# Performance work log

Measured on AMD Instinct MI355X. Metric: run time of the kernel, lower is better.

The kernel has to match this reference:

```python
import jax, jax.numpy as jnp
import numpy as np

N = 4096
D_IMG = 512
D_FEAT = 512
D_H = 256
D_Z = 128
N_CLS = 64
CHANGE_FRAC = 1.0  # alpha


def setup_inputs() -> dict:
    key = jax.random.key(0)
    ks = jax.random.split(key, 12)
    u = jax.random.uniform(ks[0], (N, N))
    a = (jnp.triu(u, 1) < 0.01).astype(jnp.float32)
    adj_ori = a + a.T
    i = jnp.arange(N)
    # GCN-normalized adjacency D^-1/2 (A+I) D^-1/2 (input to ep_net)
    a_hat = adj_ori.at[i, i].set(1.0)
    d = jnp.power(a_hat.sum(1), -0.5)
    adj_norm = a_hat * d[:, None] * d[None, :]
    xav = lambda k, s: jax.random.uniform(k, s, jnp.float32, -1.0, 1.0) * jnp.sqrt(6.0 / (s[0] + s[1]))
    return {
        "adj_norm": adj_norm,
        "adj_ori": adj_ori,
        "feats_ori": jax.random.normal(ks[1], (N, D_FEAT), jnp.float32),
        "img_feats": jax.random.normal(ks[2], (N, D_IMG), jnp.float32),
        "csd_ori": jax.random.normal(ks[3], (N_CLS, D_FEAT), jnp.float32),
        "csd_img": jax.random.normal(ks[4], (N_CLS, D_IMG), jnp.float32),
        "noise": jax.random.normal(ks[5], (N, D_Z), jnp.float32),
        "Wb": xav(ks[6], (D_IMG, D_H)),
        "Wm": xav(ks[7], (D_H, D_Z)),
        "Wl": xav(ks[8], (D_H, D_Z)),
        "fc1_W": xav(ks[9], (2 * D_FEAT, D_H)),
        "fc1_b": jnp.zeros((D_H,), jnp.float32),
        "fc2_W": xav(ks[10], (2 * D_H, D_IMG)),
        "fc2_b": jnp.zeros((D_IMG,), jnp.float32),
    }


def _ceil_st(x):
    # CeilNoGradient: ceil forward, identity backward (straight-through)
    return x + jax.lax.stop_gradient(jnp.ceil(x) - x)


def _gsage_layer(adj, h, W, b, relu):
    neigh = adj @ h
    mean_neigh = neigh / (adj.sum(axis=1, keepdims=True) + 1e-7)
    x = jnp.concatenate((h, mean_neigh), axis=1) @ W + b
    return jax.nn.relu(x) if relu else x


def _sample_adj_edge(adj_logits, adj):
    n_edges = jnp.sum(adj != 0)
    n_change = jnp.floor(n_edges.astype(jnp.float32) * CHANGE_FRAC / 2.0).astype(jnp.int32)
    ep = jnp.triu(adj_logits, 1)
    ep = ep - jnp.min(ep)
    ep = ep / jnp.max(ep)
    T = N * N
    # --- remove lowest-prob existing edges ---
    mask_rm = ep * adj
    v = jnp.sort(mask_rm.reshape(-1))  # ascending; positives at the tail
    n_nz = jnp.sum(v > 0)
    n_rm = jnp.minimum(n_nz, n_change)
    thresh_rm = v[T - n_nz + n_rm - 1]  # n_rm-th smallest positive
    mask_rm = jnp.where(mask_rm > thresh_rm, 0.0, mask_rm)
    mask_rm = _ceil_st(mask_rm)
    mask_rm = mask_rm + mask_rm.T
    adj_new = adj - mask_rm
    # --- add highest-prob missing edges ---
    mask_add = ep * (1.0 - adj)
    v2 = jnp.sort(mask_add.reshape(-1))
    n_nz2 = jnp.sum(v2 > 0)
    n_add = jnp.minimum(n_nz2, n_change)
    thresh_add = v2[T - n_add]  # n_add-th largest positive
    mask_add = jnp.where(mask_add < thresh_add, 0.0, mask_add)
    mask_add = _ceil_st(mask_add)
    mask_add = mask_add + mask_add.T
    return adj_new + mask_add


def reference(adj_norm, adj_ori, feats_ori, img_feats, csd_ori, csd_img, noise,
              Wb, Wm, Wl, fc1_W, fc1_b, fc2_W, fc2_b):
    # ep_net (VGAE, gae=False)
    hidden = adj_norm @ (img_feats @ Wb)
    mean = jax.nn.relu(adj_norm @ (hidden @ Wm))
    logstd = jax.nn.relu(adj_norm @ (hidden @ Wl))
    Z = noise * jnp.exp(logstd) + mean
    adj_logits = Z @ Z.T
    # edge rewiring
    adj_new = _sample_adj_edge(adj_logits, adj_ori)
    # normalize_adj for 'gsage': fill diag 1, L1 row-normalize
    i = jnp.arange(N)
    adj_new = adj_new.at[i, i].set(1.0)
    adj_new = adj_new / jnp.maximum(jnp.sum(jnp.abs(adj_new), axis=1, keepdims=True), 1e-12)
    # nc_net (DGPN)
    preds_img = img_feats @ csd_img.T
    h1 = _gsage_layer(adj_new, feats_ori, fc1_W, fc1_b, relu=True)
    h2 = _gsage_layer(adj_new, h1, fc2_W, fc2_b, relu=False)
    feat_total = jax.nn.log_softmax(h2, axis=-1)
    preds_total = feat_total @ csd_img.T
    return preds_total, feat_total, preds_img, adj_logits
```

## Files before the change

kernel.cpp:

```cpp
#include <hip/hip_runtime.h>
#include <type_traits>
#include <stdint.h>

#define NN 4096
#define TTOT 16777216UL

enum { F_RELU=1, F_ACC=2, F_RS=4, F_BIAS=8 };

typedef unsigned short ushort_t;
using bf16x8 = __attribute__((ext_vector_type(8))) short;
using f32x4  = __attribute__((ext_vector_type(4))) float;

struct SelParams {
  unsigned min_ord, max_ord, n_up;
  float lo, M, c0;
  unsigned n_change, rm_prefix, rm_k, add_prefix, add_k;
  float t_rm, t_add;
  unsigned hist_rm[256], hist_add[256];
};

__device__ __forceinline__ unsigned ordenc(float x){
  unsigned u = __float_as_uint(x);
  return (u & 0x80000000u) ? ~u : (u | 0x80000000u);
}
__device__ __forceinline__ float orddec_ok(unsigned o){
  unsigned u = (o & 0x80000000u) ? (o ^ 0x80000000u) : ~o;
  return __uint_as_float(u);
}
__device__ __forceinline__ ushort_t f2bf(float x){
  unsigned u = __float_as_uint(x);
  return (ushort_t)((u + 0x7FFFu + ((u >> 16) & 1u)) >> 16);
}
__device__ __forceinline__ float bf2f(ushort_t h){
  return __uint_as_float(((unsigned)h) << 16);
}

template<int DN>
__global__ __launch_bounds__(256)
void k_b3t(const float* __restrict__ Bsrc, ushort_t* __restrict__ H,
           ushort_t* __restrict__ Mg, ushort_t* __restrict__ L)
{
  __shared__ ushort_t sh[64][65], sm[64][65], sl[64][65];
  const int t = threadIdx.x;
  const int n0 = blockIdx.x * 64, k0 = blockIdx.y * 64;
  #pragma unroll
  for (int it = 0; it < 16; ++it){
    int idx = it*256 + t; int r = idx >> 6, c = idx & 63;
    float x  = Bsrc[(size_t)(k0 + r)*DN + n0 + c];
    ushort_t hb = f2bf(x);
    float r1 = x - bf2f(hb);
    ushort_t mb = f2bf(r1);
    float r2 = r1 - bf2f(mb);
    ushort_t lb = f2bf(r2);
    sh[r][c] = hb; sm[r][c] = mb; sl[r][c] = lb;
  }
  __syncthreads();
  #pragma unroll
  for (int it = 0; it < 16; ++it){
    int idx = it*256 + t; int r = idx >> 6, c = idx & 63;
    size_t o = (size_t)(n0 + r)*4096 + k0 + c;
    H[o] = sh[c][r]; Mg[o] = sm[c][r]; L[o] = sl[c][r];
  }
}

__global__ __launch_bounds__(256)
void k_mfma(const signed char* __restrict__ A8,
            const ushort_t* __restrict__ BH, const ushort_t* __restrict__ BM2,
            const ushort_t* __restrict__ BL,
            float* __restrict__ C0, float* __restrict__ C1, int N)
{
  __shared__ ushort_t Ab[64][72];
  __shared__ ushort_t Bb[3][64][72];
  const int t = threadIdx.x;
  const int m0 = blockIdx.y * 64, n0 = blockIdx.x * 64;
  const int kz = blockIdx.z;
  const int kbase = kz * 2048;
  float* C = kz ? C1 : C0;
  const int sr = t >> 2, sc = (t & 3) * 16;
  const int w = t >> 6, lane = t & 63;
  const int fr = lane & 15, fg = lane >> 4;

  int4 a_r = *reinterpret_cast<const int4*>(A8 + (size_t)(m0+sr)*4096 + kbase + sc);
  const ushort_t* bsrc0 = BH  + (size_t)(n0+sr)*4096 + kbase + sc;
  const ushort_t* bsrc1 = BM2 + (size_t)(n0+sr)*4096 + kbase + sc;
  const ushort_t* bsrc2 = BL  + (size_t)(n0+sr)*4096 + kbase + sc;
  int4 b0a = reinterpret_cast<const int4*>(bsrc0)[0], b0b = reinterpret_cast<const int4*>(bsrc0)[1];
  int4 b1a = reinterpret_cast<const int4*>(bsrc1)[0], b1b = reinterpret_cast<const int4*>(bsrc1)[1];
  int4 b2a = reinterpret_cast<const int4*>(bsrc2)[0], b2b = reinterpret_cast<const int4*>(bsrc2)[1];

  f32x4 acc[4][3];
  #pragma unroll
  for (int c = 0; c < 4; ++c)
    #pragma unroll
    for (int p = 0; p < 3; ++p)
      acc[c][p] = (f32x4){0.f, 0.f, 0.f, 0.f};

  for (int k0 = 0; k0 < 2048; k0 += 64){
    {
      alignas(16) ushort_t tmp[16];
      const signed char* ab = reinterpret_cast<const signed char*>(&a_r);
      #pragma unroll
      for (int i = 0; i < 16; ++i) tmp[i] = f2bf((float)(int)ab[i]);
      *reinterpret_cast<int4*>(&Ab[sr][sc])     = reinterpret_cast<int4*>(tmp)[0];
      *reinterpret_cast<int4*>(&Ab[sr][sc + 8]) = reinterpret_cast<int4*>(tmp)[1];
      *reinterpret_cast<int4*>(&Bb[0][sr][sc])     = b0a;
      *reinterpret_cast<int4*>(&Bb[0][sr][sc + 8]) = b0b;
      *reinterpret_cast<int4*>(&Bb[1][sr][sc])     = b1a;
      *reinterpret_cast<int4*>(&Bb[1][sr][sc + 8]) = b1b;
      *reinterpret_cast<int4*>(&Bb[2][sr][sc])     = b2a;
      *reinterpret_cast<int4*>(&Bb[2][sr][sc + 8]) = b2b;
    }
    __syncthreads();
    if (k0 + 64 < 2048){
      a_r = *reinterpret_cast<const int4*>(A8 + (size_t)(m0+sr)*4096 + kbase + (k0+64) + sc);
      const ushort_t* p0 = BH  + (size_t)(n0+sr)*4096 + kbase + (k0+64) + sc;
      const ushort_t* p1 = BM2 + (size_t)(n0+sr)*4096 + kbase + (k0+64) + sc;
      const ushort_t* p2 = BL  + (size_t)(n0+sr)*4096 + kbase + (k0+64) + sc;
      b0a = reinterpret_cast<const int4*>(p0)[0]; b0b = reinterpret_cast<const int4*>(p0)[1];
      b1a = reinterpret_cast<const int4*>(p1)[0]; b1b = reinterpret_cast<const int4*>(p1)[1];
      b2a = reinterpret_cast<const int4*>(p2)[0]; b2b = reinterpret_cast<const int4*>(p2)[1];
    }
    #pragma unroll
    for (int kk = 0; kk < 64; kk += 32){
      bf16x8 af = *reinterpret_cast<const bf16x8*>(&Ab[w*16 + fr][kk + fg*8]);
      #pragma unroll
      for (int c = 0; c < 4; ++c){
        const int bn = c*16 + fr;
        bf16x8 bh = *reinterpret_cast<const bf16x8*>(&Bb[0][bn][kk + fg*8]);
        acc[c][0] = __builtin_amdgcn_mfma_f32_16x16x32_bf16(af, bh, acc[c][0], 0, 0, 0);
        bf16x8 bm = *reinterpret_cast<const bf16x8*>(&Bb[1][bn][kk + fg*8]);
        acc[c][1] = __builtin_amdgcn_mfma_f32_16x16x32_bf16(af, bm, acc[c][1], 0, 0, 0);
        bf16x8 bl = *reinterpret_cast<const bf16x8*>(&Bb[2][bn][kk + fg*8]);
        acc[c][2] = __builtin_amdgcn_mfma_f32_16x16x32_bf16(af, bl, acc[c][2], 0, 0, 0);
      }
    }
    __syncthreads();
  }
  #pragma unroll
  for (int c = 0; c < 4; ++c){
    f32x4 s = acc[c][0] + acc[c][1];
    s = s + acc[c][2];
    #pragma unroll
    for (int r = 0; r < 4; ++r)
      C[(size_t)(m0 + w*16 + fg*4 + r)*N + n0 + c*16 + fr] = s[r];
  }
}

__global__ __launch_bounds__(256)
void k_add2(const float* __restrict__ A, const float* __restrict__ B,
            float* __restrict__ O, int n4)
{
  int i = blockIdx.x*256 + threadIdx.x;
  if (i < n4){
    float4 a = reinterpret_cast<const float4*>(A)[i];
    float4 b = reinterpret_cast<const float4*>(B)[i];
    reinterpret_cast<float4*>(O)[i] = make_float4(a.x+b.x, a.y+b.y, a.z+b.z, a.w+b.w);
  }
}

__global__ __launch_bounds__(256)
void k_z2p(const float* __restrict__ MPLP, const float* __restrict__ noise,
           ushort_t* __restrict__ ZH, ushort_t* __restrict__ ZM,
           ushort_t* __restrict__ ZL)
{
  int i = blockIdx.x*256 + threadIdx.x;
  int m = i >> 7, c = i & 127;
  float mp = fmaxf(MPLP[(size_t)m*256 + c], 0.0f);
  float lp = fmaxf(MPLP[(size_t)m*256 + 128 + c], 0.0f);
  float z = noise[i]*expf(lp) + mp;
  ushort_t hb = f2bf(z);
  float r1 = z - bf2f(hb);
  ushort_t mb = f2bf(r1);
  float r2 = r1 - bf2f(mb);
  ushort_t lb = f2bf(r2);
  ZH[i] = hb; ZM[i] = mb; ZL[i] = lb;
}

__global__ __launch_bounds__(256)
void k_zztm(const ushort_t* __restrict__ ZH, const ushort_t* __restrict__ ZM,
            const ushort_t* __restrict__ ZL, float* __restrict__ C)
{
  const int bx = blockIdx.x, by = blockIdx.y;
  if (by > bx) return;
  __shared__ float Cs[64][68];
  const int t = threadIdx.x;
  const int m0 = by*64, n0 = bx*64;
  const int w = t >> 6, lane = t & 63;
  const int fr = lane & 15, fg = lane >> 4;
  const int arow = m0 + w*16 + fr;

  f32x4 acc[4];
  #pragma unroll
  for (int c = 0; c < 4; ++c) acc[c] = (f32x4){0.f,0.f,0.f,0.f};

  #pragma unroll
  for (int kk = 0; kk < 128; kk += 32){
    bf16x8 ah = *reinterpret_cast<const bf16x8*>(ZH + (size_t)arow*128 + kk + fg*8);
    bf16x8 am = *reinterpret_cast<const bf16x8*>(ZM + (size_t)arow*128 + kk + fg*8);
    bf16x8 al = *reinterpret_cast<const bf16x8*>(ZL + (size_t)arow*128 + kk + fg*8);
    #pragma unroll
    for (int c = 0; c < 4; ++c){
      const int brow = n0 + c*16 + fr;
      bf16x8 bh = *reinterpret_cast<const bf16x8*>(ZH + (size_t)brow*128 + kk + fg*8);
      bf16x8 bm = *reinterpret_cast<const bf16x8*>(ZM + (size_t)brow*128 + kk + fg*8);
      bf16x8 bl = *reinterpret_cast<const bf16x8*>(ZL + (size_t)brow*128 + kk + fg*8);
      acc[c] = __builtin_amdgcn_mfma_f32_16x16x32_bf16(ah, bh, acc[c], 0, 0, 0);
      acc[c] = __builtin_amdgcn_mfma_f32_16x16x32_bf16(ah, bm, acc[c], 0, 0, 0);
      acc[c] = __builtin_amdgcn_mfma_f32_16x16x32_bf16(am, bh, acc[c], 0, 0, 0);
      acc[c] = __builtin_amdgcn_mfma_f32_16x16x32_bf16(ah, bl, acc[c], 0, 0, 0);
      acc[c] = __builtin_amdgcn_mfma_f32_16x16x32_bf16(al, bh, acc[c], 0, 0, 0);
      acc[c] = __builtin_amdgcn_mfma_f32_16x16x32_bf16(am, bm, acc[c], 0, 0, 0);
    }
  }
  #pragma unroll
  for (int c = 0; c < 4; ++c)
    #pragma unroll
    for (int r = 0; r < 4; ++r)
      Cs[w*16 + fg*4 + r][c*16 + fr] = acc[c][r];
  __syncthreads();
  const int rr = t >> 2, cb = (t & 3) * 16;
  #pragma unroll
  for (int j = 0; j < 4; ++j){
    float4 v = *reinterpret_cast<const float4*>(&Cs[rr][cb + j*4]);
    *reinterpret_cast<float4*>(&C[(size_t)(m0+rr)*NN + n0 + cb + j*4]) = v;
  }
  if (bx != by){
    #pragma unroll
    for (int j = 0; j < 4; ++j){
      float4 v = make_float4(Cs[cb+j*4+0][rr], Cs[cb+j*4+1][rr],
                             Cs[cb+j*4+2][rr], Cs[cb+j*4+3][rr]);
      *reinterpret_cast<float4*>(&C[(size_t)(n0+rr)*NN + m0 + cb + j*4]) = v;
    }
  }
}

template<typename TA>
__global__ __launch_bounds__(256)
void k_gemm32(const TA* __restrict__ A, const float* __restrict__ B,
              float* __restrict__ C, int M, int N, int K, int ldc,
              const float* __restrict__ rowscale, const float* __restrict__ bias,
              int flags)
{
  __shared__ float As[16][36];
  __shared__ float Bs[16][68];
  const int t  = threadIdx.x;
  const int tx = t & 15, ty = t >> 4;
  const int m0 = blockIdx.y * 32, n0 = blockIdx.x * 64;
  float acc[2][4] = {};
  for (int k0 = 0; k0 < K; k0 += 16) {
    if (t < 128){
      const int mA = t >> 2, kA = (t & 3) * 4;
      if constexpr (std::is_same<TA, float>::value) {
        float4 v = *reinterpret_cast<const float4*>(A + (size_t)(m0+mA)*K + (k0+kA));
        As[kA+0][mA]=v.x; As[kA+1][mA]=v.y; As[kA+2][mA]=v.z; As[kA+3][mA]=v.w;
      } else {
        int u = *reinterpret_cast<const int*>(A + (size_t)(m0+mA)*K + (k0+kA));
        As[kA+0][mA]=(float)(int)(signed char)( u       & 0xff);
        As[kA+1][mA]=(float)(int)(signed char)((u>>8)   & 0xff);
        As[kA+2][mA]=(float)(int)(signed char)((u>>16)  & 0xff);
        As[kA+3][mA]=(float)(int)(signed char)((u>>24)  & 0xff);
      }
    }
    {
      const int kB = t >> 4, nB = (t & 15) * 4;
      float4 w = *reinterpret_cast<const float4*>(B + (size_t)(k0+kB)*N + (n0+nB));
      Bs[kB][nB+0]=w.x; Bs[kB][nB+1]=w.y; Bs[kB][nB+2]=w.z; Bs[kB][nB+3]=w.w;
    }
    __syncthreads();
    #pragma unroll
    for (int kk = 0; kk < 16; ++kk) {
      float a0 = As[kk][ty*2+0];
      float a1 = As[kk][ty*2+1];
      float4 bv = *reinterpret_cast<const float4*>(&Bs[kk][tx*4]);
      float b[4]={bv.x,bv.y,bv.z,bv.w};
      #pragma unroll
      for (int j=0;j<4;++j){
        acc[0][j] = fmaf(a0, b[j], acc[0][j]);
        acc[1][j] = fmaf(a1, b[j], acc[1][j]);
      }
    }
    __syncthreads();
  }
  #pragma unroll
  for (int i=0;i<2;++i){
    const int m = m0 + ty*2 + i;
    const float rsv = (flags & F_RS) ? rowscale[m] : 1.0f;
    float* cp = C + (size_t)m*ldc + (n0 + tx*4);
    float o[4];
    #pragma unroll
    for (int j=0;j<4;++j){
      float v = acc[i][j] * rsv;
      if (flags & F_BIAS) v += bias[n0 + tx*4 + j];
      if (flags & F_ACC)  v += cp[j];
      if (flags & F_RELU) v = fmaxf(v, 0.0f);
      o[j] = v;
    }
    *reinterpret_cast<float4*>(cp) = make_float4(o[0],o[1],o[2],o[3]);
  }
}

__global__ __launch_bounds__(256)
void k_gemm32T(const float* __restrict__ A, const float* __restrict__ B,
               float* __restrict__ C, int M, int N, int K, int ldc)
{
  __shared__ float As[16][36];
  __shared__ float Bs[16][68];
  const int t  = threadIdx.x;
  const int tx = t & 15, ty = t >> 4;
  const int m0 = blockIdx.y * 32, n0 = blockIdx.x * 64;
  float acc[2][4] = {};
  for (int k0 = 0; k0 < K; k0 += 16) {
    if (t < 128){
      const int mA = t >> 2, kA = (t & 3) * 4;
      float4 v = *reinterpret_cast<const float4*>(A + (size_t)(m0+mA)*K + (k0+kA));
      As[kA+0][mA]=v.x; As[kA+1][mA]=v.y; As[kA+2][mA]=v.z; As[kA+3][mA]=v.w;
    }
    {
      const int nB = t >> 2, kB = (t & 3) * 4;
      float4 w = *reinterpret_cast<const float4*>(B + (size_t)(n0+nB)*K + (k0+kB));
      Bs[kB+0][nB]=w.x; Bs[kB+1][nB]=w.y; Bs[kB+2][nB]=w.z; Bs[kB+3][nB]=w.w;
    }
    __syncthreads();
    #pragma unroll
    for (int kk = 0; kk < 16; ++kk) {
      float a0 = As[kk][ty*2+0];
      float a1 = As[kk][ty*2+1];
      float4 bv = *reinterpret_cast<const float4*>(&Bs[kk][tx*4]);
      float b[4]={bv.x,bv.y,bv.z,bv.w};
      #pragma unroll
      for (int j=0;j<4;++j){
        acc[0][j] = fmaf(a0, b[j], acc[0][j]);
        acc[1][j] = fmaf(a1, b[j], acc[1][j]);
      }
    }
    __syncthreads();
  }
  #pragma unroll
  for (int i=0;i<2;++i){
    const int m = m0 + ty*2 + i;
    float* cp = C + (size_t)m*ldc + (n0 + tx*4);
    *reinterpret_cast<float4*>(cp) = make_float4(acc[i][0],acc[i][1],acc[i][2],acc[i][3]);
  }
}

__global__ __launch_bounds__(256)
void k_fc(const float* __restrict__ A1, const float* __restrict__ B1,
          const float* __restrict__ bias,
          const float* __restrict__ A2, const float* __restrict__ B2,
          const float* __restrict__ rowscale,
          float* __restrict__ C, int N, int K1, int K2, int relu)
{
  __shared__ float As[16][36];
  __shared__ float Bs[16][68];
  const int t  = threadIdx.x;
  const int tx = t & 15, ty = t >> 4;
  const int m0 = blockIdx.y * 32, n0 = blockIdx.x * 64;
  float acc1[2][4] = {};
  float acc2[2][4] = {};
  for (int k0 = 0; k0 < K1; k0 += 16) {
    if (t < 128){
      const int mA = t >> 2, kA = (t & 3) * 4;
      float4 v = *reinterpret_cast<const float4*>(A1 + (size_t)(m0+mA)*K1 + (k0+kA));
      As[kA+0][mA]=v.x; As[kA+1][mA]=v.y; As[kA+2][mA]=v.z; As[kA+3][mA]=v.w;
    }
    {
      const int kB = t >> 4, nB = (t & 15) * 4;
      float4 w = *reinterpret_cast<const float4*>(B1 + (size_t)(k0+kB)*N + (n0+nB));
      Bs[kB][nB+0]=w.x; Bs[kB][nB+1]=w.y; Bs[kB][nB+2]=w.z; Bs[kB][nB+3]=w.w;
    }
    __syncthreads();
    #pragma unroll
    for (int kk = 0; kk < 16; ++kk) {
      float a0 = As[kk][ty*2+0];
      float a1 = As[kk][ty*2+1];
      float4 bv = *reinterpret_cast<const float4*>(&Bs[kk][tx*4]);
      float b[4]={bv.x,bv.y,bv.z,bv.w};
      #pragma unroll
      for (int j=0;j<4;++j){
        acc1[0][j] = fmaf(a0, b[j], acc1[0][j]);
        acc1[1][j] = fmaf(a1, b[j], acc1[1][j]);
      }
    }
    __syncthreads();
  }
  for (int k0 = 0; k0 < K2; k0 += 16) {
    if (t < 128){
      const int mA = t >> 2, kA = (t & 3) * 4;
      float4 v = *reinterpret_cast<const float4*>(A2 + (size_t)(m0+mA)*K2 + (k0+kA));
      As[kA+0][mA]=v.x; As[kA+1][mA]=v.y; As[kA+2][mA]=v.z; As[kA+3][mA]=v.w;
    }
    {
      const int kB = t >> 4, nB = (t & 15) * 4;
      float4 w = *reinterpret_cast<const float4*>(B2 + (size_t)(k0+kB)*N + (n0+nB));
      Bs[kB][nB+0]=w.x; Bs[kB][nB+1]=w.y; Bs[kB][nB+2]=w.z; Bs[kB][nB+3]=w.w;
    }
    __syncthreads();
    #pragma unroll
    for (int kk = 0; kk < 16; ++kk) {
      float a0 = As[kk][ty*2+0];
      float a1 = As[kk][ty*2+1];
      float4 bv = *reinterpret_cast<const float4*>(&Bs[kk][tx*4]);
      float b[4]={bv.x,bv.y,bv.z,bv.w};
      #pragma unroll
      for (int j=0;j<4;++j){
        acc2[0][j] = fmaf(a0, b[j], acc2[0][j]);
        acc2[1][j] = fmaf(a1, b[j], acc2[1][j]);
      }
    }
    __syncthreads();
  }
  #pragma unroll
  for (int i=0;i<2;++i){
    const int m = m0 + ty*2 + i;
    const float rsv = rowscale[m];
    float* cp = C + (size_t)m*N + (n0 + tx*4);
    float o[4];
    #pragma unroll
    for (int j=0;j<4;++j){
      float t1 = acc1[i][j] + bias[n0 + tx*4 + j];
      float v  = acc2[i][j] * rsv;
      v += t1;
      if (relu) v = fmaxf(v, 0.0f);
      o[j] = v;
    }
    *reinterpret_cast<float4*>(cp) = make_float4(o[0],o[1],o[2],o[3]);
  }
}

__global__ __launch_bounds__(256)
void k_wcat(const float* __restrict__ Wm, const float* __restrict__ Wl,
            float* __restrict__ Wcat)
{
  int idx = blockIdx.x*256 + threadIdx.x;
  int row = idx >> 8, col = idx & 255;
  Wcat[idx] = (col < 128) ? Wm[row*128 + col] : Wl[row*128 + (col - 128)];
}

template<int D>
__global__ __launch_bounds__(256)
void k_spmmF(const float* __restrict__ A, const float* __restrict__ B,
             float* __restrict__ C)
{
  const int row = blockIdx.x, t = threadIdx.x;
  const int lane = t & 63, wv = t >> 6;
  __shared__ int   sc[288];
  __shared__ float sv[288];
  __shared__ int wtot[4];
  __shared__ int nsh;
  const float4* r4 = reinterpret_cast<const float4*>(A + (size_t)row*NN) + t*4;
  float lv[16];
  #pragma unroll
  for (int q=0;q<4;++q){
    float4 v = r4[q];
    lv[q*4+0]=v.x; lv[q*4+1]=v.y; lv[q*4+2]=v.z; lv[q*4+3]=v.w;
  }
  int c = 0;
  #pragma unroll
  for (int k=0;k<16;++k) c += (lv[k] != 0.0f);
  int inc = c;
  #pragma unroll
  for (int off=1; off<64; off<<=1){
    int v = __shfl_up(inc, off, 64);
    if (lane >= off) inc += v;
  }
  if (lane == 63) wtot[wv] = inc;
  __syncthreads();
  int wbase = 0;
  #pragma unroll
  for (int ww=0; ww<3; ++ww) if (ww < wv) wbase += wtot[ww];
  int pos = wbase + inc - c;
  #pragma unroll
  for (int k=0;k<16;++k){
    if (lv[k] != 0.0f){
      if (pos >= 0 && pos < 288){ sc[pos] = t*16+k; sv[pos] = lv[k]; }
      pos++;
    }
  }
  if (t == 255){
    int tot = wbase + inc;
    nsh = (tot < 288) ? tot : 288;
  }
  __syncthreads();
  const int n = nsh;
  float acc = 0.f;
  int s = 0;
  for (; s+4 <= n; s += 4){
    float x0 = B[(size_t)sc[s+0]*D + t];
    float x1 = B[(size_t)sc[s+1]*D + t];
    float x2 = B[(size_t)sc[s+2]*D + t];
    float x3 = B[(size_t)sc[s+3]*D + t];
    acc = fmaf(sv[s+0], x0, acc);
    acc = fmaf(sv[s+1], x1, acc);
    acc = fmaf(sv[s+2], x2, acc);
    acc = fmaf(sv[s+3], x3, acc);
  }
  for (; s < n; ++s) acc = fmaf(sv[s], B[(size_t)sc[s]*D + t], acc);
  C[(size_t)row*D + t] = acc;
}

__global__ __launch_bounds__(256)
void k_initstats(SelParams* p)
{
  int t = threadIdx.x;
  if (t == 0){
    p->min_ord = 0xFFFFFFFFu; p->max_ord = 0u; p->n_up = 0u;
    p->rm_prefix = 0u; p->add_prefix = 0u;
  }
  p->hist_rm[t] = 0u; p->hist_add[t] = 0u;
}

__global__ __launch_bounds__(256)
void k_stats1(const float* __restrict__ L, const float* __restrict__ adj,
              unsigned long long* __restrict__ mask, SelParams* __restrict__ p)
{
  unsigned mn=0xFFFFFFFFu, mx=0u, cnt=0u;
  size_t g = (size_t)blockIdx.x*256 + threadIdx.x;
  const size_t stride = (size_t)gridDim.x*256;
  for (; g < 262144; g += stride){
    const int i  = (int)(g >> 6);
    const int jb = (int)(g & 63) << 6;
    unsigned long long m = 0ull;
    if (jb + 63 > i){
      const float4* a4 = reinterpret_cast<const float4*>(adj + (size_t)i*NN + jb);
      const float4* l4 = reinterpret_cast<const float4*>(L   + (size_t)i*NN + jb);
      for (int w = 0; w < 16; ++w){
        const int j0 = jb + w*4;
        if (j0 + 3 <= i) continue;
        float4 av = a4[w]; float4 lv = l4[w];
        float ae[4]={av.x,av.y,av.z,av.w};
        float le[4]={lv.x,lv.y,lv.z,lv.w};
        #pragma unroll
        for (int e=0;e<4;++e){
          const int jj = j0 + e;
          if (jj > i){
            if (ae[e] != 0.0f){ m |= 1ull << (jj & 63); cnt++; }
            unsigned o = ordenc(le[e]);
            mn = (o < mn) ? o : mn;
            mx = (o > mx) ? o : mx;
          }
        }
      }
    }
    mask[g] = m;
  }
  __shared__ unsigned smn[256], smx[256], sc[256];
  int t = threadIdx.x;
  smn[t]=mn; smx[t]=mx; sc[t]=cnt; __syncthreads();
  for (int s=128; s>0; s>>=1){
    if (t < s){
      smn[t] = (smn[t+s] < smn[t]) ? smn[t+s] : smn[t];
      smx[t] = (smx[t+s] > smx[t]) ? smx[t+s] : smx[t];
      sc[t] += sc[t+s];
    }
    __syncthreads();
  }
  if (t == 0){
    atomicMin(&p->min_ord, smn[0]);
    atomicMax(&p->max_ord, smx[0]);
    atomicAdd(&p->n_up, sc[0]);
  }
}

__global__ void k_stats2(SelParams* p)
{
  float mnv = orddec_ok(p->min_ord), mxv = orddec_ok(p->max_ord);
  float lo = fminf(mnv, 0.0f), hi = fmaxf(mxv, 0.0f);
  p->lo = lo;
  p->M  = hi - lo;
  p->c0 = (0.0f - lo) / p->M;
  p->n_change = p->n_up;
}

__global__ __launch_bounds__(256)
void k_hist2(const float* __restrict__ L, const unsigned long long* __restrict__ mask,
             SelParams* __restrict__ p, int shift)
{
  __shared__ unsigned hr[256], ha[256];
  const int t = threadIdx.x;
  hr[t]=0u; ha[t]=0u; __syncthreads();
  const float lo = p->lo, Mv = p->M;
  const unsigned pr = p->rm_prefix, pa = p->add_prefix;
  const float4* L4 = reinterpret_cast<const float4*>(L);
  size_t q = (size_t)blockIdx.x*256 + t;
  const size_t stride = (size_t)gridDim.x*256;
  for (; q < TTOT/4; q += stride){
    const int i = (int)(q >> 10);
    const int j = (int)(q & 1023) << 2;
    if (j + 3 <= i) continue;
    float4 l = L4[q];
    const unsigned long long w = mask[q >> 4];
    float le[4]={l.x,l.y,l.z,l.w};
    #pragma unroll
    for (int e=0;e<4;++e){
      const int jj = j + e;
      if (jj <= i) continue;
      const unsigned key = __float_as_uint((le[e] - lo) / Mv);
      if (key == 0u) continue;
      const bool edge = (w >> (jj & 63)) & 1ull;
      if (edge){
        if (shift == 24 || (key >> (shift+8)) == pr) atomicAdd(&hr[(key>>shift)&255u], 1u);
      } else {
        if (shift == 24 || (key >> (shift+8)) == pa) atomicAdd(&ha[(key>>shift)&255u], 1u);
      }
    }
  }
  __syncthreads();
  if (hr[t]) atomicAdd(&p->hist_rm[t], hr[t]);
  if (ha[t]) atomicAdd(&p->hist_add[t], ha[t]);
}

__global__ __launch_bounds__(256)
void k_scan2(SelParams* __restrict__ p, int shift)
{
  const int t = threadIdx.x;
  if (t == 0){
    const unsigned c0k  = __float_as_uint(p->c0);
    const unsigned n_up = p->n_up;
    {
      unsigned injb = 300u, inj = 0u;
      if (c0k != 0u && (shift == 24 || (c0k >> (shift+8)) == p->rm_prefix)){
        injb = (c0k >> shift) & 255u; inj = n_up;
      }
      unsigned k;
      if (shift == 24){
        unsigned tot = inj;
        for (int d=0; d<256; ++d) tot += p->hist_rm[d];
        k = (tot < p->n_change) ? tot : p->n_change;
      } else k = p->rm_k;
      unsigned cum = 0u, digit = 255u;
      for (int d=0; d<256; ++d){
        unsigned hd = p->hist_rm[d] + (((unsigned)d == injb) ? inj : 0u);
        if (cum + hd >= k){ digit = (unsigned)d; k -= cum; break; }
        cum += hd;
      }
      p->rm_prefix = (p->rm_prefix << 8) | digit;
      p->rm_k = k;
      if (shift == 0) p->t_rm = __uint_as_float(p->rm_prefix);
    }
    {
      unsigned injb = 300u, inj = 0u;
      if (c0k != 0u && (shift == 24 || (c0k >> (shift+8)) == p->add_prefix)){
        injb = (c0k >> shift) & 255u;
        inj  = 8386560u - n_up + 4096u;
      }
      unsigned k;
      if (shift == 24){
        unsigned tot = inj;
        for (int d=0; d<256; ++d) tot += p->hist_add[d];
        k = (tot < p->n_change) ? tot : p->n_change;
      } else k = p->add_k;
      unsigned cum = 0u, digit = 0u;
      for (int d=255; d>=0; --d){
        unsigned hd = p->hist_add[d] + (((unsigned)d == injb) ? inj : 0u);
        if (cum + hd >= k){ digit = (unsigned)d; k -= cum; break; }
        cum += hd;
      }
      p->add_prefix = (p->add_prefix << 8) | digit;
      p->add_k = k;
      if (shift == 0) p->t_add = __uint_as_float(p->add_prefix);
    }
  }
  __syncthreads();
  p->hist_rm[t] = 0u; p->hist_add[t] = 0u;
}

__device__ __forceinline__ int adjval(bool edge, float v, float c0v, float trm, float tad)
{
  int rmU = (edge && v   >  0.0f && v   <= trm) ? 1 : 0;
  int rmL = (edge && c0v >  0.0f && c0v <= trm) ? 1 : 0;
  int adU = (!edge && v   >= tad) ? 1 : 0;
  int adL = (!edge && c0v >= tad) ? 1 : 0;
  return (edge ? 1 : 0) - rmU - rmL + adU + adL;
}

__global__ __launch_bounds__(256)
void k_apply(const float* __restrict__ L, const unsigned long long* __restrict__ mask,
             const SelParams* __restrict__ p, signed char* __restrict__ A8)
{
  const int bx = blockIdx.x, by = blockIdx.y;
  if (by > bx) return;
  const float lo=p->lo, Mv=p->M, c0v=p->c0, trm=p->t_rm, tad=p->t_add;
  const int i0 = by*64, j0 = bx*64, t = threadIdx.x;
  __shared__ signed char Vs[64][65];
  if (bx == by){
    for (int it=0; it<16; ++it){
      int e = it*256 + t; int r = e>>6, c = e&63;
      size_t idx = (size_t)(i0+r)*NN + (j0+c);
      if (r < c){
        bool edge = (mask[idx>>6] >> ((j0+c) & 63)) & 1ull;
        float v = (L[idx] - lo) / Mv;
        int val = adjval(edge, v, c0v, trm, tad);
        A8[idx] = (signed char)val;
        Vs[c][r] = (signed char)val;
      } else if (r == c){
        A8[idx] = 1;
      }
    }
    __syncthreads();
    for (int it=0; it<16; ++it){
      int e = it*256 + t; int r = e>>6, c = e&63;
      if (r > c) A8[(size_t)(i0+r)*NN + (j0+c)] = Vs[r][c];
    }
  } else {
    for (int it=0; it<16; ++it){
      int e = it*256 + t; int r = e>>6, c = e&63;
      size_t idx = (size_t)(i0+r)*NN + (j0+c);
      bool edge = (mask[idx>>6] >> ((j0+c) & 63)) & 1ull;
      float v = (L[idx] - lo) / Mv;
      int val = adjval(edge, v, c0v, trm, tad);
      A8[idx] = (signed char)val;
      Vs[c][r] = (signed char)val;
    }
    __syncthreads();
    for (int it=0; it<16; ++it){
      int e = it*256 + t; int r = e>>6, c = e&63;
      A8[(size_t)(j0+r)*NN + (i0+c)] = Vs[r][c];
    }
  }
}

__global__ __launch_bounds__(256)
void k_rowsum8(const signed char* __restrict__ A8, float* __restrict__ s_mean)
{
  const int row = blockIdx.x, t = threadIdx.x;
  const int4 w = reinterpret_cast<const int4*>(A8 + (size_t)row*NN)[t];
  int s = 0, a = 0;
  int vs[4] = {w.x, w.y, w.z, w.w};
  #pragma unroll
  for (int q=0; q<4; ++q){
    int u = vs[q];
    #pragma unroll
    for (int b=0; b<4; ++b){
      int c = (int)(signed char)((u >> (8*b)) & 0xff);
      s += c; a += (c < 0) ? -c : c;
    }
  }
  __shared__ int rs_[256], ra_[256];
  rs_[t]=s; ra_[t]=a; __syncthreads();
  for (int st=128; st>0; st>>=1){
    if (t < st){ rs_[t]+=rs_[t+st]; ra_[t]+=ra_[t+st]; }
    __syncthreads();
  }
  if (t == 0){
    float rs = (float)rs_[0], ra = (float)ra_[0];
    float A = fmaxf(ra, 1e-12f);
    s_mean[row] = (1.0f / A) / (rs / A + 1e-7f);
  }
}

__global__ __launch_bounds__(256)
void k_lsm(float* __restrict__ X)
{
  const int row = blockIdx.x, t = threadIdx.x;
  float* x = X + (size_t)row*512;
  float v0 = x[t], v1 = x[t+256];
  __shared__ float red[256];
  red[t] = fmaxf(v0, v1); __syncthreads();
  for (int s=128; s>0; s>>=1){
    if (t < s) red[t] = fmaxf(red[t], red[t+s]);
    __syncthreads();
  }
  float m = red[0]; __syncthreads();
  red[t] = expf(v0-m) + expf(v1-m); __syncthreads();
  for (int s=128; s>0; s>>=1){
    if (t < s) red[t] += red[t+s];
    __syncthreads();
  }
  float ls = logf(red[0]);
  x[t]     = (v0 - m) - ls;
  x[t+256] = (v1 - m) - ls;
}

extern "C" void kernel_launch(void* const* d_in, const int* in_sizes, int n_in,
                              void* d_out, int out_size, void* d_ws, size_t ws_size,
                              hipStream_t stream)
{
  (void)in_sizes; (void)n_in; (void)out_size; (void)ws_size;
  const float* adj_norm = (const float*)d_in[0];
  const float* adj_ori  = (const float*)d_in[1];
  const float* feats    = (const float*)d_in[2];
  const float* img      = (const float*)d_in[3];
  const float* csd_img  = (const float*)d_in[5];
  const float* noise    = (const float*)d_in[6];
  const float* Wb       = (const float*)d_in[7];
  const float* Wm       = (const float*)d_in[8];
  const float* Wl       = (const float*)d_in[9];
  const float* fc1W     = (const float*)d_in[10];
  const float* fc1b     = (const float*)d_in[11];
  const float* fc2W     = (const float*)d_in[12];
  const float* fc2b     = (const float*)d_in[13];

  float* out    = (float*)d_out;
  float* out_pt = out;
  float* out_ft = out + 262144;
  float* out_pi = out + 2359296;
  float* out_lg = out + 2621440;

  char* W = (char*)d_ws;
  signed char* adj8 = (signed char*)W;
  float* bufA   = (float*)(W + (16u<<20));
  float* bufB   = (float*)(W + (24u<<20));
  float* HMHL   = (float*)(W + (28u<<20));
  float* MPLP   = (float*)(W + (32u<<20));
  unsigned long long* mask = (unsigned long long*)(W + (38u<<20));
  float* p2q0   = (float*)(W + (40u<<20));
  float* s_mean = (float*)(W + (44u<<20));
  SelParams* sp = (SelParams*)(W + (44u<<20) + 65536);
  float* Wcat   = (float*)(W + (45u<<20));
  ushort_t* ZH = (ushort_t*)(W + (40u<<20));
  ushort_t* ZM = (ushort_t*)(W + (41u<<20));
  ushort_t* ZL = (ushort_t*)(W + (42u<<20));
  ushort_t* BT1h = (ushort_t*)(W + (28u<<20));
  ushort_t* BT1m = (ushort_t*)(W + (32u<<20));
  ushort_t* BT1l = (ushort_t*)(W + (36u<<20));
  ushort_t* BT2h = (ushort_t*)(W + (28u<<20));
  ushort_t* BT2m = (ushort_t*)(W + (30u<<20));
  ushort_t* BT2l = (ushort_t*)(W + (32u<<20));

  dim3 B(256);
  auto G32 = [](int M, int N){ return dim3((unsigned)(N/64), (unsigned)(M/32)); };

  k_gemm32<float><<<G32(4096,256),B,0,stream>>>(img, Wb, bufA, 4096,256,512,256, nullptr,nullptr,0);
  k_spmmF<256><<<4096,B,0,stream>>>(adj_norm, bufA, bufB);
  k_wcat<<<256,B,0,stream>>>(Wm, Wl, Wcat);
  k_gemm32<float><<<G32(4096,256),B,0,stream>>>(bufB, Wcat, HMHL, 4096,256,256,256, nullptr,nullptr,0);
  k_spmmF<256><<<4096,B,0,stream>>>(adj_norm, HMHL, MPLP);
  k_z2p<<<2048,B,0,stream>>>(MPLP, noise, ZH, ZM, ZL);
  k_zztm<<<dim3(64,64),B,0,stream>>>(ZH, ZM, ZL, out_lg);

  k_initstats<<<1,B,0,stream>>>(sp);
  k_stats1<<<1024,B,0,stream>>>(out_lg, adj_ori, mask, sp);
  k_stats2<<<1,1,0,stream>>>(sp);
  for (int shift = 24; shift >= 0; shift -= 8){
    k_hist2<<<2048,B,0,stream>>>(out_lg, mask, sp, shift);
    k_scan2<<<1,B,0,stream>>>(sp, shift);
  }
  k_apply<<<dim3(64,64),B,0,stream>>>(out_lg, mask, sp, adj8);

  k_rowsum8<<<4096,B,0,stream>>>(adj8, s_mean);

  k_b3t<512><<<dim3(8,64),B,0,stream>>>(feats, BT1h, BT1m, BT1l);
  k_mfma<<<dim3(8,64,2),B,0,stream>>>(adj8, BT1h, BT1m, BT1l, bufA, out_ft, 512);
  k_add2<<<2048,B,0,stream>>>(bufA, out_ft, bufA, 524288);
  k_fc<<<G32(4096,256),B,0,stream>>>(feats, fc1W, fc1b, bufA, fc1W + 512*256, s_mean,
                                     bufB, 256, 512, 512, 1);
  k_b3t<256><<<dim3(4,64),B,0,stream>>>(bufB, BT2h, BT2m, BT2l);
  k_mfma<<<dim3(4,64,2),B,0,stream>>>(adj8, BT2h, BT2m, BT2l, p2q0, out_ft, 256);
  k_add2<<<1024,B,0,stream>>>(p2q0, out_ft, bufA, 262144);
  k_fc<<<G32(4096,512),B,0,stream>>>(bufB, fc2W, fc2b, bufA, fc2W + 256*512, s_mean,
                                     out_ft, 512, 256, 256, 0);
  k_lsm<<<4096,B,0,stream>>>(out_ft);

  k_gemm32T<<<G32(4096,64),B,0,stream>>>(out_ft, csd_img, out_pt, 4096,64,512,64);
  k_gemm32T<<<G32(4096,64),B,0,stream>>>(img, csd_img, out_pi, 4096,64,512,64);
}
```

Measured before the change: 906.1 us.

## Stage Z tiles in LDS for ZZ^T and swap warp-to-tile mapping in adj GEMM

The Z·Zᵀ logits kernel now cooperatively loads the 64-row A and B tiles of the three bf16 split components into shared memory, instead of having each wave read B fragments straight from global memory. The epilogue reuses that shared buffer for the transpose stage. The adjacency MFMA kernel swaps its mapping so each wave holds one B column fragment and loops over four A row tiles, which cuts LDS fragment loads per iteration (3 B + 4 A instead of 1 A + 12 B). Both changes aim to reduce redundant memory traffic, at the cost of extra shared memory and barriers in the logits kernel.

Measured after the change: 840.9 us. 1.08x faster.

```diff
diff --git a/kernel.cpp b/kernel.cpp
--- a/kernel.cpp
+++ b/kernel.cpp
@@ -90,10 +90,10 @@
 
   f32x4 acc[4][3];
   #pragma unroll
-  for (int c = 0; c < 4; ++c)
+  for (int mt = 0; mt < 4; ++mt)
     #pragma unroll
     for (int p = 0; p < 3; ++p)
-      acc[c][p] = (f32x4){0.f, 0.f, 0.f, 0.f};
+      acc[mt][p] = (f32x4){0.f, 0.f, 0.f, 0.f};
 
   for (int k0 = 0; k0 < 2048; k0 += 64){
     {
@@ -122,27 +122,27 @@
     }
     #pragma unroll
     for (int kk = 0; kk < 64; kk += 32){
-      bf16x8 af = *reinterpret_cast<const bf16x8*>(&Ab[w*16 + fr][kk + fg*8]);
+      const int bn = w*16 + fr;
+      bf16x8 bh = *reinterpret_cast<const bf16x8*>(&Bb[0][bn][kk + fg*8]);
+      bf16x8 bm = *reinterpret_cast<const bf16x8*>(&Bb[1][bn][kk + fg*8]);
+      bf16x8 bl = *reinterpret_cast<const bf16x8*>(&Bb[2][bn][kk + fg*8]);
       #pragma unroll
-      for (int c = 0; c < 4; ++c){
-        const int bn = c*16 + fr;
-        bf16x8 bh = *reinterpret_cast<const bf16x8*>(&Bb[0][bn][kk + fg*8]);
-        acc[c][0] = __builtin_amdgcn_mfma_f32_16x16x32_bf16(af, bh, acc[c][0], 0, 0, 0);
-        bf16x8 bm = *reinterpret_cast<const bf16x8*>(&Bb[1][bn][kk + fg*8]);
-        acc[c][1] = __builtin_amdgcn_mfma_f32_16x16x32_bf16(af, bm, acc[c][1], 0, 0, 0);
-        bf16x8 bl = *reinterpret_cast<const bf16x8*>(&Bb[2][bn][kk + fg*8]);
-        acc[c][2] = __builtin_amdgcn_mfma_f32_16x16x32_bf16(af, bl, acc[c][2], 0, 0, 0);
-      }
-    }
-    __syncthreads();
-  }
-  #pragma unroll
-  for (int c = 0; c < 4; ++c){
-    f32x4 s = acc[c][0] + acc[c][1];
-    s = s + acc[c][2];
+      for (int mt = 0; mt < 4; ++mt){
+        bf16x8 af = *reinterpret_cast<const bf16x8*>(&Ab[mt*16 + fr][kk + fg*8]);
+        acc[mt][0] = __builtin_amdgcn_mfma_f32_16x16x32_bf16(af, bh, acc[mt][0], 0, 0, 0);
+        acc[mt][1] = __builtin_amdgcn_mfma_f32_16x16x32_bf16(af, bm, acc[mt][1], 0, 0, 0);
+        acc[mt][2] = __builtin_amdgcn_mfma_f32_16x16x32_bf16(af, bl, acc[mt][2], 0, 0, 0);
+      }
+    }
+    __syncthreads();
+  }
+  #pragma unroll
+  for (int mt = 0; mt < 4; ++mt){
+    f32x4 s = acc[mt][0] + acc[mt][1];
+    s = s + acc[mt][2];
     #pragma unroll
     for (int r = 0; r < 4; ++r)
-      C[(size_t)(m0 + w*16 + fg*4 + r)*N + n0 + c*16 + fr] = s[r];
+      C[(size_t)(m0 + mt*16 + fg*4 + r)*N + n0 + w*16 + fr] = s[r];
   }
 }
 
@@ -177,58 +177,89 @@
 }
 
 __global__ __launch_bounds__(256)
-void k_zztm(const ushort_t* __restrict__ ZH, const ushort_t* __restrict__ ZM,
-            const ushort_t* __restrict__ ZL, float* __restrict__ C)
+void k_zztm2(const ushort_t* __restrict__ ZH, const ushort_t* __restrict__ ZM,
+             const ushort_t* __restrict__ ZL, float* __restrict__ C)
 {
   const int bx = blockIdx.x, by = blockIdx.y;
   if (by > bx) return;
-  __shared__ float Cs[64][68];
+  __shared__ ushort_t As[3][64][72];
+  __shared__ ushort_t Bs[3][64][72];
   const int t = threadIdx.x;
   const int m0 = by*64, n0 = bx*64;
+  const int sr = t >> 2, sc = (t & 3) * 16;
   const int w = t >> 6, lane = t & 63;
   const int fr = lane & 15, fg = lane >> 4;
-  const int arow = m0 + w*16 + fr;
 
   f32x4 acc[4];
   #pragma unroll
-  for (int c = 0; c < 4; ++c) acc[c] = (f32x4){0.f,0.f,0.f,0.f};
-
-  #pragma unroll
-  for (int kk = 0; kk < 128; kk += 32){
-    bf16x8 ah = *reinterpret_cast<const bf16x8*>(ZH + (size_t)arow*128 + kk + fg*8);
-    bf16x8 am = *reinterpret_cast<const bf16x8*>(ZM + (size_t)arow*128 + kk + fg*8);
-    bf16x8 al = *reinterpret_cast<const bf16x8*>(ZL + (size_t)arow*128 + kk + fg*8);
-    #pragma unroll
-    for (int c = 0; c < 4; ++c){
-      const int brow = n0 + c*16 + fr;
-      bf16x8 bh = *reinterpret_cast<const bf16x8*>(ZH + (size_t)brow*128 + kk + fg*8);
-      bf16x8 bm = *reinterpret_cast<const bf16x8*>(ZM + (size_t)brow*128 + kk + fg*8);
-      bf16x8 bl = *reinterpret_cast<const bf16x8*>(ZL + (size_t)brow*128 + kk + fg*8);
-      acc[c] = __builtin_amdgcn_mfma_f32_16x16x32_bf16(ah, bh, acc[c], 0, 0, 0);
-      acc[c] = __builtin_amdgcn_mfma_f32_16x16x32_bf16(ah, bm, acc[c], 0, 0, 0);
-      acc[c] = __builtin_amdgcn_mfma_f32_16x16x32_bf16(am, bh, acc[c], 0, 0, 0);
-      acc[c] = __builtin_amdgcn_mfma_f32_16x16x32_bf16(ah, bl, acc[c], 0, 0, 0);
-      acc[c] = __builtin_amdgcn_mfma_f32_16x16x32_bf16(al, bh, acc[c], 0, 0, 0);
-      acc[c] = __builtin_amdgcn_mfma_f32_16x16x32_bf16(am, bm, acc[c], 0, 0, 0);
-    }
-  }
-  #pragma unroll
-  for (int c = 0; c < 4; ++c)
+  for (int mt = 0; mt < 4; ++mt) acc[mt] = (f32x4){0.f,0.f,0.f,0.f};
+
+  for (int k0 = 0; k0 < 128; k0 += 64){
+    const ushort_t* pa0 = ZH + (size_t)(m0+sr)*128 + k0 + sc;
+    const ushort_t* pa1 = ZM + (size_t)(m0+sr)*128 + k0 + sc;
+    const ushort_t* pa2 = ZL + (size_t)(m0+sr)*128 + k0 + sc;
+    const ushort_t* pb0 = ZH + (size_t)(n0+sr)*128 + k0 + sc;
+    const ushort_t* pb1 = ZM + (size_t)(n0+sr)*128 + k0 + sc;
+    const ushort_t* pb2 = ZL + (size_t)(n0+sr)*128 + k0 + sc;
+    int4 a0a = reinterpret_cast<const int4*>(pa0)[0], a0b = reinterpret_cast<const int4*>(pa0)[1];
+    int4 a1a = reinterpret_cast<const int4*>(pa1)[0], a1b = reinterpret_cast<const int4*>(pa1)[1];
+    int4 a2a = reinterpret_cast<const int4*>(pa2)[0], a2b = reinterpret_cast<const int4*>(pa2)[1];
+    int4 b0a = reinterpret_cast<const int4*>(pb0)[0], b0b = reinterpret_cast<const int4*>(pb0)[1];
+    int4 b1a = reinterpret_cast<const int4*>(pb1)[0], b1b = reinterpret_cast<const int4*>(pb1)[1];
+    int4 b2a = reinterpret_cast<const int4*>(pb2)[0], b2b = reinterpret_cast<const int4*>(pb2)[1];
+    __syncthreads();
+    *reinterpret_cast<int4*>(&As[0][sr][sc])     = a0a;
+    *reinterpret_cast<int4*>(&As[0][sr][sc + 8]) = a0b;
+    *reinterpret_cast<int4*>(&As[1][sr][sc])     = a1a;
+    *reinterpret_cast<int4*>(&As[1][sr][sc + 8]) = a1b;
+    *reinterpret_cast<int4*>(&As[2][sr][sc])     = a2a;
+    *reinterpret_cast<int4*>(&As[2][sr][sc + 8]) = a2b;
+    *reinterpret_cast<int4*>(&Bs[0][sr][sc])     = b0a;
+    *reinterpret_cast<int4*>(&Bs[0][sr][sc + 8]) = b0b;
+    *reinterpret_cast<int4*>(&Bs[1][sr][sc])     = b1a;
+    *reinterpret_cast<int4*>(&Bs[1][sr][sc + 8]) = b1b;
+    *reinterpret_cast<int4*>(&Bs[2][sr][sc])     = b2a;
+    *reinterpret_cast<int4*>(&Bs[2][sr][sc + 8]) = b2b;
+    __syncthreads();
+    #pragma unroll
+    for (int kk = 0; kk < 64; kk += 32){
+      const int bn = w*16 + fr;
+      bf16x8 bh = *reinterpret_cast<const bf16x8*>(&Bs[0][bn][kk + fg*8]);
+      bf16x8 bm = *reinterpret_cast<const bf16x8*>(&Bs[1][bn][kk + fg*8]);
+      bf16x8 bl = *reinterpret_cast<const bf16x8*>(&Bs[2][bn][kk + fg*8]);
+      #pragma unroll
+      for (int mt = 0; mt < 4; ++mt){
+        bf16x8 ah = *reinterpret_cast<const bf16x8*>(&As[0][mt*16 + fr][kk + fg*8]);
+        bf16x8 am = *reinterpret_cast<const bf16x8*>(&As[1][mt*16 + fr][kk + fg*8]);
+        bf16x8 al = *reinterpret_cast<const bf16x8*>(&As[2][mt*16 + fr][kk + fg*8]);
+        acc[mt] = __builtin_amdgcn_mfma_f32_16x16x32_bf16(ah, bh, acc[mt], 0, 0, 0);
+        acc[mt] = __builtin_amdgcn_mfma_f32_16x16x32_bf16(ah, bm, acc[mt], 0, 0, 0);
+        acc[mt] = __builtin_amdgcn_mfma_f32_16x16x32_bf16(am, bh, acc[mt], 0, 0, 0);
+        acc[mt] = __builtin_amdgcn_mfma_f32_16x16x32_bf16(ah, bl, acc[mt], 0, 0, 0);
+        acc[mt] = __builtin_amdgcn_mfma_f32_16x16x32_bf16(al, bh, acc[mt], 0, 0, 0);
+        acc[mt] = __builtin_amdgcn_mfma_f32_16x16x32_bf16(am, bm, acc[mt], 0, 0, 0);
+      }
+    }
+  }
+  __syncthreads();
+  float* Cs = reinterpret_cast<float*>(As);
+  #pragma unroll
+  for (int mt = 0; mt < 4; ++mt)
     #pragma unroll
     for (int r = 0; r < 4; ++r)
-      Cs[w*16 + fg*4 + r][c*16 + fr] = acc[c][r];
+      Cs[(mt*16 + fg*4 + r)*68 + w*16 + fr] = acc[mt][r];
   __syncthreads();
   const int rr = t >> 2, cb = (t & 3) * 16;
   #pragma unroll
   for (int j = 0; j < 4; ++j){
-    float4 v = *reinterpret_cast<const float4*>(&Cs[rr][cb + j*4]);
+    float4 v = *reinterpret_cast<const float4*>(&Cs[rr*68 + cb + j*4]);
     *reinterpret_cast<float4*>(&C[(size_t)(m0+rr)*NN + n0 + cb + j*4]) = v;
   }
   if (bx != by){
     #pragma unroll
     for (int j = 0; j < 4; ++j){
-      float4 v = make_float4(Cs[cb+j*4+0][rr], Cs[cb+j*4+1][rr],
-                             Cs[cb+j*4+2][rr], Cs[cb+j*4+3][rr]);
+      float4 v = make_float4(Cs[(cb+j*4+0)*68 + rr], Cs[(cb+j*4+1)*68 + rr],
+                             Cs[(cb+j*4+2)*68 + rr], Cs[(cb+j*4+3)*68 + rr]);
       *reinterpret_cast<float4*>(&C[(size_t)(n0+rr)*NN + m0 + cb + j*4]) = v;
     }
   }
@@ -826,7 +857,7 @@
   k_gemm32<float><<<G32(4096,256),B,0,stream>>>(bufB, Wcat, HMHL, 4096,256,256,256, nullptr,nullptr,0);
   k_spmmF<256><<<4096,B,0,stream>>>(adj_norm, HMHL, MPLP);
   k_z2p<<<2048,B,0,stream>>>(MPLP, noise, ZH, ZM, ZL);
-  k_zztm<<<dim3(64,64),B,0,stream>>>(ZH, ZM, ZL, out_lg);
+  k_zztm2<<<dim3(64,64),B,0,stream>>>(ZH, ZM, ZL, out_lg);
 
   k_initstats<<<1,B,0,stream>>>(sp);
   k_stats1<<<1024,B,0,stream>>>(out_lg, adj_ori, mask, sp);
```
